# Optimization experiments

Measured on AMD Instinct MI355X. Metric: run time of the kernel, lower is better.

Reference implementation:

```python
import jax, jax.numpy as jnp
import numpy as np

N = 50000      # nodes
E = 800000     # edges (before self-loops)
F_IN = 256
H = 8          # heads layer 1
C = 64         # hidden channels per head
OUT = 40       # classes
NEG_SLOPE = 0.2


def setup_inputs() -> dict:
    key = jax.random.key(0)
    ks = jax.random.split(key, 10)
    sc = 0.05
    return {
        "x": jax.random.normal(ks[0], (N, F_IN), jnp.float32),
        "edge_index": jax.random.randint(ks[1], (2, E), 0, N, dtype=jnp.int64),
        "W1": jax.random.normal(ks[2], (F_IN, H * C), jnp.float32) * sc,
        "a_src1": jax.random.normal(ks[3], (H, C), jnp.float32) * sc,
        "a_dst1": jax.random.normal(ks[4], (H, C), jnp.float32) * sc,
        "b1": jnp.zeros((H * C,), jnp.float32),
        "W2": jax.random.normal(ks[5], (H * C, OUT), jnp.float32) * sc,
        "a_src2": jax.random.normal(ks[6], (1, OUT), jnp.float32) * sc,
        "a_dst2": jax.random.normal(ks[7], (1, OUT), jnp.float32) * sc,
        "b2": jnp.zeros((OUT,), jnp.float32),
    }


def gat_layer(h_in, src, dst, W, a_s, a_d, b, heads, ch, concat, n):
    # h: [n, heads, ch] per-head linear transform
    h = (h_in @ W).reshape(n, heads, ch)
    alpha_s = jnp.sum(h * a_s, axis=-1)   # [n, heads]
    alpha_d = jnp.sum(h * a_d, axis=-1)   # [n, heads]
    # edge-wise raw attention logits [E, heads]
    e = jax.nn.leaky_relu(alpha_s[src] + alpha_d[dst], NEG_SLOPE)
    # segment softmax over incoming edges of each dst node
    m = jax.ops.segment_max(e, dst, num_segments=n)
    w = jnp.exp(e - m[dst])
    s = jax.ops.segment_sum(w, dst, num_segments=n)
    alpha = w / s[dst]                    # [E, heads]
    # scatter-aggregate messages: [n, heads, ch]
    out = jax.ops.segment_sum(h[src] * alpha[:, :, None], dst, num_segments=n)
    out = out.reshape(n, heads * ch) if concat else out.mean(axis=1)
    return out + b


def reference(x, edge_index, W1, a_src1, a_dst1, b1, W2, a_src2, a_dst2, b2):
    # add self-loops (PyG GATConv default); guarantees every dst has >=1 edge
    loop = jnp.arange(N, dtype=edge_index.dtype)
    src = jnp.concatenate([edge_index[0], loop])
    dst = jnp.concatenate([edge_index[1], loop])
    h = gat_layer(x, src, dst, W1, a_src1, a_dst1, b1, H, C, True, N)
    h = jax.nn.relu(h)  # dropout is identity in eval mode
    out = gat_layer(h, src, dst, W2, a_src2, a_dst2, b2, 1, OUT, False, N)
    return jax.nn.log_softmax(out, axis=1)
```

## Files before the change

kernel.cpp:

```cpp
#include <hip/hip_runtime.h>

#define N_NODES 50000
#define N_EDGES 800000
#define F_INK   256
#define HC      512
#define OUT_C   40
#define OUT_P   48
#define NEG     0.2f
#define CAP     64
#define GEMM_NB 782
#define CHUNKS  782
#define PART_SZ 6250
#define SCAT_NB (CHUNKS * 8)

typedef short short8 __attribute__((ext_vector_type(8)));
typedef float f32x4 __attribute__((ext_vector_type(4)));
typedef float f32x2 __attribute__((ext_vector_type(2)));

__device__ __forceinline__ float bf2f(unsigned short u) {
    union { unsigned int i; float f; } v; v.i = ((unsigned int)u) << 16; return v.f;
}
__device__ __forceinline__ unsigned short f2bf(float f) {
    union { float f; unsigned int i; } v; v.f = f;
    unsigned int x = v.i;
    return (unsigned short)((x + 0x7fffu + ((x >> 16) & 1u)) >> 16);
}
__device__ __forceinline__ float bflo(unsigned int u) {
    union { unsigned int i; float f; } v; v.i = u << 16; return v.f;
}
__device__ __forceinline__ float bfhi(unsigned int u) {
    union { unsigned int i; float f; } v; v.i = u & 0xffff0000u; return v.f;
}
__device__ __forceinline__ bool ei_is64(const int* ei) {
    return ei[1] == 0 && ei[3] == 0 && ei[5] == 0;
}
__device__ __forceinline__ float lrelu(float x) { return fmaxf(x, NEG * x); }
__device__ __forceinline__ unsigned char f2fp8(float v) {
    return (unsigned char)(__builtin_amdgcn_cvt_pk_fp8_f32(v, v, 0, false) & 0xff);
}
__device__ __forceinline__ float fp82f(unsigned char b) {
    f32x2 p = __builtin_amdgcn_cvt_pk_f32_fp8((int)b, false);
    return p[0];
}

__global__ __launch_bounds__(256) void prep_k(const float* __restrict__ W1, const float* __restrict__ W2,
                       const float* __restrict__ s1, const float* __restrict__ d1, const float* __restrict__ b1,
                       const float* __restrict__ s2, const float* __restrict__ d2, const float* __restrict__ b2,
                       unsigned short* __restrict__ W1p, unsigned short* __restrict__ W2p,
                       unsigned short* __restrict__ s1c, unsigned short* __restrict__ d1c,
                       unsigned short* __restrict__ b1c, unsigned short* __restrict__ s2c,
                       unsigned short* __restrict__ d2c, unsigned short* __restrict__ b2c,
                       int* __restrict__ cnt) {
    int b = blockIdx.x;
    if (b < 512) {
        int t = b * 256 + threadIdx.x;
        int k = t / HC, n = t % HC;
        int s = k >> 5, q = (k >> 3) & 3, j = k & 7;
        W1p[((((s << 2) + q) * HC + n) << 3) + j] = f2bf(W1[k * HC + n]);
    } else if (b < 608) {
        int t = (b - 512) * 256 + threadIdx.x;
        int k = t / OUT_P, n = t % OUT_P;
        int s = k >> 5, q = (k >> 3) & 3, j = k & 7;
        unsigned short v = (n < OUT_C) ? f2bf(W2[k * OUT_C + n]) : (unsigned short)0;
        W2p[((((s << 2) + q) * OUT_P + n) << 3) + j] = v;
    } else if (b == 608) {
        int t = threadIdx.x;
        for (int j = t; j < 512; j += 256) {
            s1c[j] = f2bf(s1[j]); d1c[j] = f2bf(d1[j]); b1c[j] = f2bf(b1[j]);
        }
        if (t < OUT_C) { s2c[t] = f2bf(s2[t]); d2c[t] = f2bf(d2[t]); b2c[t] = f2bf(b2[t]); }
    } else {
        int i = (b - 609) * 256 + threadIdx.x;
        if (i < N_NODES) cnt[i * 16] = 0;
    }
}

__global__ __launch_bounds__(256) void gemm1_k(const float* __restrict__ x,
                                               const unsigned short* __restrict__ Wp,
                                               const unsigned short* __restrict__ a_s,
                                               const unsigned short* __restrict__ a_d,
                                               unsigned char* __restrict__ h1f8,
                                               float* __restrict__ as1, float* __restrict__ ad1,
                                               const int* __restrict__ ei,
                                               int* __restrict__ cnt, int* __restrict__ srcs) {
    __shared__ unsigned short xs[64 * 264];
    int tid = threadIdx.x;
    if (blockIdx.x >= GEMM_NB) {
        int sb = blockIdx.x - GEMM_NB;
        int part = blockIdx.x & 7;
        int chunk = sb >> 3;
        int lo = part * PART_SZ;
        bool is64 = ei_is64(ei);
        int e0 = chunk * 1024 + (tid << 2);
        int s[4], d[4];
        bool vld[4];
        if (chunk < CHUNKS - 1) {
            if (is64) {
                int4 a0 = *reinterpret_cast<const int4*>(ei + 2 * e0);
                int4 a1 = *reinterpret_cast<const int4*>(ei + 2 * e0 + 4);
                int4 c0 = *reinterpret_cast<const int4*>(ei + 2 * N_EDGES + 2 * e0);
                int4 c1 = *reinterpret_cast<const int4*>(ei + 2 * N_EDGES + 2 * e0 + 4);
                s[0] = a0.x; s[1] = a0.z; s[2] = a1.x; s[3] = a1.z;
                d[0] = c0.x; d[1] = c0.z; d[2] = c1.x; d[3] = c1.z;
            } else {
                int4 a0 = *reinterpret_cast<const int4*>(ei + e0);
                int4 c0 = *reinterpret_cast<const int4*>(ei + N_EDGES + e0);
                s[0] = a0.x; s[1] = a0.y; s[2] = a0.z; s[3] = a0.w;
                d[0] = c0.x; d[1] = c0.y; d[2] = c0.z; d[3] = c0.w;
            }
            vld[0] = vld[1] = vld[2] = vld[3] = true;
        } else {
#pragma unroll
            for (int j = 0; j < 4; j++) {
                int e = e0 + j;
                vld[j] = e < N_EDGES;
                int ec = vld[j] ? e : 0;
                s[j] = is64 ? ei[2 * ec] : ei[ec];
                d[j] = is64 ? ei[2 * N_EDGES + 2 * ec] : ei[N_EDGES + ec];
            }
        }
#pragma unroll
        for (int j = 0; j < 4; j++) {
            int dj = d[j];
            if (vld[j] && dj >= lo && dj < lo + PART_SZ) {
                int pos = atomicAdd(&cnt[dj * 16], 1);
                if (pos < CAP) srcs[(size_t)dj * CAP + pos] = s[j];
            }
        }
        return;
    }
    int bm = blockIdx.x;
    int row0 = bm * 64;
#pragma unroll
    for (int it = 0; it < 16; it++) {
        int j = tid + it * 256;
        int r = j >> 6;
        int c = (j & 63) << 2;
        int rr = row0 + r; rr = rr < N_NODES ? rr : N_NODES - 1;
        float4 f = *reinterpret_cast<const float4*>(x + (size_t)rr * F_INK + c);
        unsigned int lo = (unsigned int)f2bf(f.x) | ((unsigned int)f2bf(f.y) << 16);
        unsigned int hi = (unsigned int)f2bf(f.z) | ((unsigned int)f2bf(f.w) << 16);
        *reinterpret_cast<uint2*>(&xs[r * 264 + c]) = make_uint2(lo, hi);
    }
    __syncthreads();
    int w = tid >> 6, lane = tid & 63;
    int q = lane >> 4, l16 = lane & 15;
    short8 a[8];
#pragma unroll
    for (int s = 0; s < 8; s++)
        a[s] = *reinterpret_cast<const short8*>(&xs[(w * 16 + l16) * 264 + s * 32 + q * 8]);
    int orow = row0 + w * 16 + q * 4;
#pragma unroll
    for (int bn = 0; bn < 8; bn++) {
        f32x4 acc[4];
#pragma unroll
        for (int t = 0; t < 4; t++) acc[t] = (f32x4){0.f, 0.f, 0.f, 0.f};
#pragma unroll
        for (int s = 0; s < 8; s++) {
#pragma unroll
            for (int t = 0; t < 4; t++) {
                int col = bn * 64 + t * 16 + l16;
                short8 b = *reinterpret_cast<const short8*>(Wp + ((((s << 2) + q) * HC + col) << 3));
                acc[t] = __builtin_amdgcn_mfma_f32_16x16x32_bf16(a[s], b, acc[t], 0, 0, 0);
            }
        }
        float sa0 = 0.f, sa1 = 0.f, sa2 = 0.f, sa3 = 0.f;
        float da0 = 0.f, da1 = 0.f, da2 = 0.f, da3 = 0.f;
#pragma unroll
        for (int t = 0; t < 4; t++) {
            int col = bn * 64 + t * 16 + l16;
            float asc = bf2f(a_s[col]);
            float adc = bf2f(a_d[col]);
            float v0 = acc[t][0], v1 = acc[t][1], v2 = acc[t][2], v3 = acc[t][3];
            sa0 += v0 * asc; da0 += v0 * adc;
            sa1 += v1 * asc; da1 += v1 * adc;
            sa2 += v2 * asc; da2 += v2 * adc;
            sa3 += v3 * asc; da3 += v3 * adc;
            if (orow + 3 < N_NODES) {
                h1f8[(size_t)(orow + 0) * HC + col] = f2fp8(v0);
                h1f8[(size_t)(orow + 1) * HC + col] = f2fp8(v1);
                h1f8[(size_t)(orow + 2) * HC + col] = f2fp8(v2);
                h1f8[(size_t)(orow + 3) * HC + col] = f2fp8(v3);
            } else {
                if (orow + 0 < N_NODES) h1f8[(size_t)(orow + 0) * HC + col] = f2fp8(v0);
                if (orow + 1 < N_NODES) h1f8[(size_t)(orow + 1) * HC + col] = f2fp8(v1);
                if (orow + 2 < N_NODES) h1f8[(size_t)(orow + 2) * HC + col] = f2fp8(v2);
                if (orow + 3 < N_NODES) h1f8[(size_t)(orow + 3) * HC + col] = f2fp8(v3);
            }
        }
#pragma unroll
        for (int m = 1; m < 16; m <<= 1) {
            sa0 += __shfl_xor(sa0, m, 64); sa1 += __shfl_xor(sa1, m, 64);
            sa2 += __shfl_xor(sa2, m, 64); sa3 += __shfl_xor(sa3, m, 64);
            da0 += __shfl_xor(da0, m, 64); da1 += __shfl_xor(da1, m, 64);
            da2 += __shfl_xor(da2, m, 64); da3 += __shfl_xor(da3, m, 64);
        }
        if (l16 < 4) {
            int rr = orow + l16;
            float sav = (l16 == 0) ? sa0 : (l16 == 1) ? sa1 : (l16 == 2) ? sa2 : sa3;
            float dav = (l16 == 0) ? da0 : (l16 == 1) ? da1 : (l16 == 2) ? da2 : da3;
            if (rr < N_NODES) { as1[rr * 8 + bn] = sav; ad1[rr * 8 + bn] = dav; }
        }
    }
}

#define ACC16(u, wgt)                                                              \
    {                                                                              \
        f32x2 q0 = __builtin_amdgcn_cvt_pk_f32_fp8((int)(u).x, false);             \
        f32x2 q1 = __builtin_amdgcn_cvt_pk_f32_fp8((int)(u).x, true);              \
        f32x2 q2 = __builtin_amdgcn_cvt_pk_f32_fp8((int)(u).y, false);             \
        f32x2 q3 = __builtin_amdgcn_cvt_pk_f32_fp8((int)(u).y, true);              \
        f32x2 q4 = __builtin_amdgcn_cvt_pk_f32_fp8((int)(u).z, false);             \
        f32x2 q5 = __builtin_amdgcn_cvt_pk_f32_fp8((int)(u).z, true);              \
        f32x2 q6 = __builtin_amdgcn_cvt_pk_f32_fp8((int)(u).w, false);             \
        f32x2 q7 = __builtin_amdgcn_cvt_pk_f32_fp8((int)(u).w, true);              \
        f32x2 wv = {(wgt), (wgt)};                                                 \
        ac[0] += wv * q0; ac[1] += wv * q1; ac[2] += wv * q2; ac[3] += wv * q3;    \
        ac[4] += wv * q4; ac[5] += wv * q5; ac[6] += wv * q6; ac[7] += wv * q7;    \
    }

__global__ __launch_bounds__(256) void agg1_k(const unsigned char* __restrict__ h1f8,
                                              const float* __restrict__ as1,
                                              const float* __restrict__ ad1,
                                              const int* __restrict__ cnt,
                                              const int* __restrict__ srcs,
                                              const unsigned short* __restrict__ b1,
                                              const unsigned short* __restrict__ W2p,
                                              const unsigned short* __restrict__ a_s2,
                                              const unsigned short* __restrict__ a_d2,
                                              unsigned char* __restrict__ h2f8) {
    __shared__ unsigned short rows[16 * 520];
    __shared__ int sSrc[16 * CAP];
    __shared__ int sCnt[16];
    __shared__ float sAs[16], sAd[16];
    __shared__ int ctr;
    int tid = threadIdx.x;
    int base = blockIdx.x * 16;
    reinterpret_cast<int4*>(sSrc)[tid] =
        reinterpret_cast<const int4*>(srcs + (size_t)base * CAP)[tid];
    if (tid < 16) {
        int d = cnt[(base + tid) * 16];
        sCnt[tid] = d < CAP ? d : CAP;
        sAs[tid] = 0.f; sAd[tid] = 0.f;
    }
    if (tid == 0) ctr = 0;
    __syncthreads();
    int w = tid >> 6, lane = tid & 63;
    int half = lane >> 5, li = lane & 31;
    int h = li >> 2;
    uint4 ub0 = reinterpret_cast<const uint4*>(b1)[li * 2 + 0];
    uint4 ub1 = reinterpret_cast<const uint4*>(b1)[li * 2 + 1];
    for (;;) {
        int rl = 0;
        if (lane == 0) rl = atomicAdd(&ctr, 1);
        rl = __shfl(rl, 0, 64);
        if (rl >= 16) break;
        int wid = base + rl;
        float adv = ad1[wid * 8 + h];
        const int* sp = sSrc + rl * CAP;
        int deg = sCnt[rl];
        f32x2 ac[8];
#pragma unroll
        for (int k = 0; k < 8; k++) ac[k] = (f32x2){0.f, 0.f};
        float sumw = 0.f;
        {
            int s = half ? (deg > 0 ? sp[0] : wid) : wid;
            float A = as1[s * 8 + h];
            uint4 u = reinterpret_cast<const uint4*>(h1f8 + (size_t)s * HC)[li];
            float wj = (half && deg == 0) ? 0.f : __expf(lrelu(A + adv));
            sumw += wj;
            ACC16(u, wj)
        }
        int v = 1;
        for (; v + 16 <= deg; v += 16) {
            int s[8]; float A[8]; uint4 u[8];
#pragma unroll
            for (int j = 0; j < 8; j++) s[j] = sp[v + 2 * j + half];
#pragma unroll
            for (int j = 0; j < 8; j++) A[j] = as1[s[j] * 8 + h];
#pragma unroll
            for (int j = 0; j < 8; j++)
                u[j] = reinterpret_cast<const uint4*>(h1f8 + (size_t)s[j] * HC)[li];
#pragma unroll
            for (int j = 0; j < 8; j++) {
                float wj = __expf(lrelu(A[j] + adv));
                sumw += wj;
                ACC16(u[j], wj)
            }
        }
        for (; v + 8 <= deg; v += 8) {
            int s[4]; float A[4]; uint4 u[4];
#pragma unroll
            for (int j = 0; j < 4; j++) s[j] = sp[v + 2 * j + half];
#pragma unroll
            for (int j = 0; j < 4; j++) A[j] = as1[s[j] * 8 + h];
#pragma unroll
            for (int j = 0; j < 4; j++)
                u[j] = reinterpret_cast<const uint4*>(h1f8 + (size_t)s[j] * HC)[li];
#pragma unroll
            for (int j = 0; j < 4; j++) {
                float wj = __expf(lrelu(A[j] + adv));
                sumw += wj;
                ACC16(u[j], wj)
            }
        }
        for (; v + 4 <= deg; v += 4) {
            int s[2]; float A[2]; uint4 u[2];
#pragma unroll
            for (int j = 0; j < 2; j++) s[j] = sp[v + 2 * j + half];
#pragma unroll
            for (int j = 0; j < 2; j++) A[j] = as1[s[j] * 8 + h];
#pragma unroll
            for (int j = 0; j < 2; j++)
                u[j] = reinterpret_cast<const uint4*>(h1f8 + (size_t)s[j] * HC)[li];
#pragma unroll
            for (int j = 0; j < 2; j++) {
                float wj = __expf(lrelu(A[j] + adv));
                sumw += wj;
                ACC16(u[j], wj)
            }
        }
        for (; v < deg; v += 2) {
            int vv = v + half;
            bool ok = vv < deg;
            int s = ok ? sp[vv] : wid;
            float A = as1[s * 8 + h];
            uint4 u = reinterpret_cast<const uint4*>(h1f8 + (size_t)s * HC)[li];
            float wj = ok ? __expf(lrelu(A + adv)) : 0.f;
            sumw += wj;
            ACC16(u, wj)
        }
        sumw += __shfl_xor(sumw, 32, 64);
#pragma unroll
        for (int k = 0; k < 8; k++) {
            ac[k][0] += __shfl_xor(ac[k][0], 32, 64);
            ac[k][1] += __shfl_xor(ac[k][1], 32, 64);
        }
        float inv = 1.f / sumw;
        f32x2 n0 = half ? ac[4] : ac[0];
        f32x2 n1 = half ? ac[5] : ac[1];
        f32x2 n2 = half ? ac[6] : ac[2];
        f32x2 n3 = half ? ac[7] : ac[3];
        uint4 ubh = half ? ub1 : ub0;
        float o0 = fmaxf(n0[0] * inv + bflo(ubh.x), 0.f);
        float o1 = fmaxf(n0[1] * inv + bfhi(ubh.x), 0.f);
        float o2 = fmaxf(n1[0] * inv + bflo(ubh.y), 0.f);
        float o3 = fmaxf(n1[1] * inv + bfhi(ubh.y), 0.f);
        float o4 = fmaxf(n2[0] * inv + bflo(ubh.z), 0.f);
        float o5 = fmaxf(n2[1] * inv + bfhi(ubh.z), 0.f);
        float o6 = fmaxf(n3[0] * inv + bflo(ubh.w), 0.f);
        float o7 = fmaxf(n3[1] * inv + bfhi(ubh.w), 0.f);
        uint4 r;
        r.x = (unsigned int)f2bf(o0) | ((unsigned int)f2bf(o1) << 16);
        r.y = (unsigned int)f2bf(o2) | ((unsigned int)f2bf(o3) << 16);
        r.z = (unsigned int)f2bf(o4) | ((unsigned int)f2bf(o5) << 16);
        r.w = (unsigned int)f2bf(o6) | ((unsigned int)f2bf(o7) << 16);
        *reinterpret_cast<uint4*>(&rows[rl * 520 + li * 16 + half * 8]) = r;
    }
    __syncthreads();
    if (w < 3) {
        int q = lane >> 4, l16 = lane & 15;
        int col = w * 16 + l16;
        f32x4 acc = (f32x4){0.f, 0.f, 0.f, 0.f};
#pragma unroll
        for (int s = 0; s < HC / 32; s++) {
            short8 a = *reinterpret_cast<const short8*>(&rows[l16 * 520 + s * 32 + q * 8]);
            short8 b = *reinterpret_cast<const short8*>(W2p + ((((s << 2) + q) * OUT_P + col) << 3));
            acc = __builtin_amdgcn_mfma_f32_16x16x32_bf16(a, b, acc, 0, 0, 0);
        }
        float sa0 = 0.f, sa1 = 0.f, sa2 = 0.f, sa3 = 0.f;
        float da0 = 0.f, da1 = 0.f, da2 = 0.f, da3 = 0.f;
        if (col < OUT_C) {
            float asc = bf2f(a_s2[col]);
            float adc = bf2f(a_d2[col]);
            sa0 = acc[0] * asc; da0 = acc[0] * adc;
            sa1 = acc[1] * asc; da1 = acc[1] * adc;
            sa2 = acc[2] * asc; da2 = acc[2] * adc;
            sa3 = acc[3] * asc; da3 = acc[3] * adc;
#pragma unroll
            for (int r = 0; r < 4; r++)
                h2f8[(size_t)(base + q * 4 + r) * 64 + col] = f2fp8(acc[r]);
        }
#pragma unroll
        for (int m = 1; m < 16; m <<= 1) {
            sa0 += __shfl_xor(sa0, m, 64); sa1 += __shfl_xor(sa1, m, 64);
            sa2 += __shfl_xor(sa2, m, 64); sa3 += __shfl_xor(sa3, m, 64);
            da0 += __shfl_xor(da0, m, 64); da1 += __shfl_xor(da1, m, 64);
            da2 += __shfl_xor(da2, m, 64); da3 += __shfl_xor(da3, m, 64);
        }
        if (l16 < 4) {
            int rr = q * 4 + l16;
            float sav = (l16 == 0) ? sa0 : (l16 == 1) ? sa1 : (l16 == 2) ? sa2 : sa3;
            float dav = (l16 == 0) ? da0 : (l16 == 1) ? da1 : (l16 == 2) ? da2 : da3;
            atomicAdd(&sAs[rr], sav);
            atomicAdd(&sAd[rr], dav);
        }
    }
    __syncthreads();
    if (tid < 16) {
        unsigned char* r = h2f8 + (size_t)(base + tid) * 64;
        *reinterpret_cast<float*>(r + 40) = sAs[tid];
        *reinterpret_cast<float*>(r + 44) = sAd[tid];
    }
}

__global__ __launch_bounds__(256) void agg2_k(const unsigned char* __restrict__ h2f8,
                                              const int* __restrict__ cnt,
                                              const int* __restrict__ srcs,
                                              const unsigned short* __restrict__ b2,
                                              float* __restrict__ outp) {
    int wid = blockIdx.x * 4 + (threadIdx.x >> 6);
    if (wid >= N_NODES) return;
    int lane = threadIdx.x & 63;
    bool act = lane < OUT_C;
    int lclamp = act ? lane : 0;
    const unsigned char* rd = h2f8 + (size_t)wid * 64;
    float adv = *reinterpret_cast<const float*>(rd + 44);
    float acc, sumw;
    {
        float w0 = __expf(lrelu(*reinterpret_cast<const float*>(rd + 40) + adv));
        sumw = w0;
        acc = w0 * fp82f(rd[lclamp]);
    }
    int deg = cnt[wid * 16]; deg = deg < CAP ? deg : CAP;
    int e = wid * CAP, e1 = e + deg;
    for (; e + 4 <= e1; e += 4) {
        int s0 = srcs[e], s1 = srcs[e + 1], s2 = srcs[e + 2], s3 = srcs[e + 3];
        const unsigned char* r0 = h2f8 + (size_t)s0 * 64;
        const unsigned char* r1 = h2f8 + (size_t)s1 * 64;
        const unsigned char* r2 = h2f8 + (size_t)s2 * 64;
        const unsigned char* r3 = h2f8 + (size_t)s3 * 64;
        float A0 = *reinterpret_cast<const float*>(r0 + 40);
        float A1 = *reinterpret_cast<const float*>(r1 + 40);
        float A2 = *reinterpret_cast<const float*>(r2 + 40);
        float A3 = *reinterpret_cast<const float*>(r3 + 40);
        unsigned char c0 = r0[lclamp];
        unsigned char c1 = r1[lclamp];
        unsigned char c2 = r2[lclamp];
        unsigned char c3 = r3[lclamp];
        float w0 = __expf(lrelu(A0 + adv));
        float w1 = __expf(lrelu(A1 + adv));
        float w2 = __expf(lrelu(A2 + adv));
        float w3 = __expf(lrelu(A3 + adv));
        sumw += (w0 + w1) + (w2 + w3);
        acc += w0 * fp82f(c0) + w1 * fp82f(c1) + w2 * fp82f(c2) + w3 * fp82f(c3);
    }
    for (; e < e1; e++) {
        int s0 = srcs[e];
        const unsigned char* r0 = h2f8 + (size_t)s0 * 64;
        float w0 = __expf(lrelu(*reinterpret_cast<const float*>(r0 + 40) + adv));
        sumw += w0;
        acc += w0 * fp82f(r0[lclamp]);
    }
    float o = acc / sumw + bf2f(b2[lclamp]);
    float mval = act ? o : -1e30f;
#pragma unroll
    for (int m = 32; m >= 1; m >>= 1) mval = fmaxf(mval, __shfl_xor(mval, m, 64));
    float ex = act ? __expf(o - mval) : 0.f;
#pragma unroll
    for (int m = 32; m >= 1; m >>= 1) ex += __shfl_xor(ex, m, 64);
    float res = o - mval - __logf(ex);
    if (act) outp[(size_t)wid * OUT_C + lane] = res;
}

extern "C" void kernel_launch(void* const* d_in, const int* in_sizes, int n_in,
                              void* d_out, int out_size, void* d_ws, size_t ws_size,
                              hipStream_t stream) {
    const float* x      = (const float*)d_in[0];
    const int*   ei     = (const int*)d_in[1];
    const float* W1     = (const float*)d_in[2];
    const float* as1raw = (const float*)d_in[3];
    const float* ad1raw = (const float*)d_in[4];
    const float* b1raw  = (const float*)d_in[5];
    const float* W2     = (const float*)d_in[6];
    const float* as2raw = (const float*)d_in[7];
    const float* ad2raw = (const float*)d_in[8];
    const float* b2raw  = (const float*)d_in[9];
    float* out = (float*)d_out;

    char* p = (char*)d_ws;
    auto alloc = [&](size_t bytes) -> char* {
        char* r = p;
        p += (bytes + 255) & ~(size_t)255;
        return r;
    };
    unsigned short* s1c  = (unsigned short*)alloc(512 * 2);
    unsigned short* d1c  = (unsigned short*)alloc(512 * 2);
    unsigned short* b1c  = (unsigned short*)alloc(512 * 2);
    unsigned short* s2c  = (unsigned short*)alloc(OUT_C * 2);
    unsigned short* d2c  = (unsigned short*)alloc(OUT_C * 2);
    unsigned short* b2c  = (unsigned short*)alloc(OUT_C * 2);
    unsigned char*  h1f8 = (unsigned char*)alloc((size_t)N_NODES * HC);
    unsigned char*  h2f8 = (unsigned char*)alloc((size_t)N_NODES * 64);
    float* as1  = (float*)alloc((size_t)N_NODES * 8 * 4);
    float* ad1  = (float*)alloc((size_t)N_NODES * 8 * 4);
    int* cnt    = (int*)alloc((size_t)N_NODES * 64);
    int* srcs   = (int*)alloc((size_t)N_NODES * CAP * 4);
    unsigned short* W1p = (unsigned short*)alloc((size_t)F_INK * HC * 2);
    unsigned short* W2p = (unsigned short*)alloc((size_t)HC * OUT_P * 2);
    (void)ws_size; (void)in_sizes; (void)n_in; (void)out_size;

    const int NB = (N_NODES + 255) / 256;

    prep_k<<<609 + NB, 256, 0, stream>>>(W1, W2, as1raw, ad1raw, b1raw, as2raw, ad2raw, b2raw,
                                         W1p, W2p, s1c, d1c, b1c, s2c, d2c, b2c, cnt);
    gemm1_k<<<GEMM_NB + SCAT_NB, 256, 0, stream>>>(x, W1p, s1c, d1c, h1f8, as1, ad1,
                                                   ei, cnt, srcs);
    agg1_k<<<N_NODES / 16, 256, 0, stream>>>(h1f8, as1, ad1, cnt, srcs, b1c,
                                             W2p, s2c, d2c, h2f8);
    agg2_k<<<(N_NODES + 3) / 4, 256, 0, stream>>>(h2f8, cnt, srcs, b2c, out);
}
```

Baseline: 273.0 us.

## Split edge scatter into its own kernel and stage source lists in LDS for agg2

Moves the edge bucketing (atomic scatter into per-destination source lists) out of the fused GEMM launch into a separate scat_k kernel, so GEMM blocks no longer share a grid with scatter blocks. The layer-2 aggregation now loads each block's four source lists and degrees into shared memory with one cooperative vectorized load, then gathers neighbor rows eight at a time to raise memory-level parallelism. The split adds a kernel launch and gives up the overlap between GEMM and scatter that the fused grid allowed.

```diff
diff --git a/kernel.cpp b/kernel.cpp
--- a/kernel.cpp
+++ b/kernel.cpp
@@ -75,60 +75,59 @@
     }
 }
 
+__global__ __launch_bounds__(256) void scat_k(const int* __restrict__ ei,
+                                              int* __restrict__ cnt, int* __restrict__ srcs) {
+    int tid = threadIdx.x;
+    int part = blockIdx.x & 7;
+    int chunk = blockIdx.x >> 3;
+    int lo = part * PART_SZ;
+    bool is64 = ei_is64(ei);
+    int e0 = chunk * 1024 + (tid << 2);
+    int s[4], d[4];
+    bool vld[4];
+    if (chunk < CHUNKS - 1) {
+        if (is64) {
+            int4 a0 = *reinterpret_cast<const int4*>(ei + 2 * e0);
+            int4 a1 = *reinterpret_cast<const int4*>(ei + 2 * e0 + 4);
+            int4 c0 = *reinterpret_cast<const int4*>(ei + 2 * N_EDGES + 2 * e0);
+            int4 c1 = *reinterpret_cast<const int4*>(ei + 2 * N_EDGES + 2 * e0 + 4);
+            s[0] = a0.x; s[1] = a0.z; s[2] = a1.x; s[3] = a1.z;
+            d[0] = c0.x; d[1] = c0.z; d[2] = c1.x; d[3] = c1.z;
+        } else {
+            int4 a0 = *reinterpret_cast<const int4*>(ei + e0);
+            int4 c0 = *reinterpret_cast<const int4*>(ei + N_EDGES + e0);
+            s[0] = a0.x; s[1] = a0.y; s[2] = a0.z; s[3] = a0.w;
+            d[0] = c0.x; d[1] = c0.y; d[2] = c0.z; d[3] = c0.w;
+        }
+        vld[0] = vld[1] = vld[2] = vld[3] = true;
+    } else {
+#pragma unroll
+        for (int j = 0; j < 4; j++) {
+            int e = e0 + j;
+            vld[j] = e < N_EDGES;
+            int ec = vld[j] ? e : 0;
+            s[j] = is64 ? ei[2 * ec] : ei[ec];
+            d[j] = is64 ? ei[2 * N_EDGES + 2 * ec] : ei[N_EDGES + ec];
+        }
+    }
+#pragma unroll
+    for (int j = 0; j < 4; j++) {
+        int dj = d[j];
+        if (vld[j] && dj >= lo && dj < lo + PART_SZ) {
+            int pos = atomicAdd(&cnt[dj * 16], 1);
+            if (pos < CAP) srcs[(size_t)dj * CAP + pos] = s[j];
+        }
+    }
+}
+
 __global__ __launch_bounds__(256) void gemm1_k(const float* __restrict__ x,
                                                const unsigned short* __restrict__ Wp,
                                                const unsigned short* __restrict__ a_s,
                                                const unsigned short* __restrict__ a_d,
                                                unsigned char* __restrict__ h1f8,
-                                               float* __restrict__ as1, float* __restrict__ ad1,
-                                               const int* __restrict__ ei,
-                                               int* __restrict__ cnt, int* __restrict__ srcs) {
+                                               float* __restrict__ as1, float* __restrict__ ad1) {
     __shared__ unsigned short xs[64 * 264];
     int tid = threadIdx.x;
-    if (blockIdx.x >= GEMM_NB) {
-        int sb = blockIdx.x - GEMM_NB;
-        int part = blockIdx.x & 7;
-        int chunk = sb >> 3;
-        int lo = part * PART_SZ;
-        bool is64 = ei_is64(ei);
-        int e0 = chunk * 1024 + (tid << 2);
-        int s[4], d[4];
-        bool vld[4];
-        if (chunk < CHUNKS - 1) {
-            if (is64) {
-                int4 a0 = *reinterpret_cast<const int4*>(ei + 2 * e0);
-                int4 a1 = *reinterpret_cast<const int4*>(ei + 2 * e0 + 4);
-                int4 c0 = *reinterpret_cast<const int4*>(ei + 2 * N_EDGES + 2 * e0);
-                int4 c1 = *reinterpret_cast<const int4*>(ei + 2 * N_EDGES + 2 * e0 + 4);
-                s[0] = a0.x; s[1] = a0.z; s[2] = a1.x; s[3] = a1.z;
-                d[0] = c0.x; d[1] = c0.z; d[2] = c1.x; d[3] = c1.z;
-            } else {
-                int4 a0 = *reinterpret_cast<const int4*>(ei + e0);
-                int4 c0 = *reinterpret_cast<const int4*>(ei + N_EDGES + e0);
-                s[0] = a0.x; s[1] = a0.y; s[2] = a0.z; s[3] = a0.w;
-                d[0] = c0.x; d[1] = c0.y; d[2] = c0.z; d[3] = c0.w;
-            }
-            vld[0] = vld[1] = vld[2] = vld[3] = true;
-        } else {
-#pragma unroll
-            for (int j = 0; j < 4; j++) {
-                int e = e0 + j;
-                vld[j] = e < N_EDGES;
-                int ec = vld[j] ? e : 0;
-                s[j] = is64 ? ei[2 * ec] : ei[ec];
-                d[j] = is64 ? ei[2 * N_EDGES + 2 * ec] : ei[N_EDGES + ec];
-            }
-        }
-#pragma unroll
-        for (int j = 0; j < 4; j++) {
-            int dj = d[j];
-            if (vld[j] && dj >= lo && dj < lo + PART_SZ) {
-                int pos = atomicAdd(&cnt[dj * 16], 1);
-                if (pos < CAP) srcs[(size_t)dj * CAP + pos] = s[j];
-            }
-        }
-        return;
-    }
     int bm = blockIdx.x;
     int row0 = bm * 64;
 #pragma unroll
@@ -409,9 +408,21 @@
                                               const int* __restrict__ srcs,
                                               const unsigned short* __restrict__ b2,
                                               float* __restrict__ outp) {
-    int wid = blockIdx.x * 4 + (threadIdx.x >> 6);
-    if (wid >= N_NODES) return;
-    int lane = threadIdx.x & 63;
+    __shared__ int sSrc[4 * CAP];
+    __shared__ int sCnt[4];
+    int tid = threadIdx.x;
+    int base = blockIdx.x * 4;
+    if (tid < 64)
+        reinterpret_cast<int4*>(sSrc)[tid] =
+            reinterpret_cast<const int4*>(srcs + (size_t)base * CAP)[tid];
+    if (tid < 4) {
+        int d = cnt[(base + tid) * 16];
+        sCnt[tid] = d < CAP ? d : CAP;
+    }
+    __syncthreads();
+    int w = tid >> 6;
+    int wid = base + w;
+    int lane = tid & 63;
     bool act = lane < OUT_C;
     int lclamp = act ? lane : 0;
     const unsigned char* rd = h2f8 + (size_t)wid * 64;
@@ -422,32 +433,45 @@
         sumw = w0;
         acc = w0 * fp82f(rd[lclamp]);
     }
-    int deg = cnt[wid * 16]; deg = deg < CAP ? deg : CAP;
-    int e = wid * CAP, e1 = e + deg;
-    for (; e + 4 <= e1; e += 4) {
-        int s0 = srcs[e], s1 = srcs[e + 1], s2 = srcs[e + 2], s3 = srcs[e + 3];
-        const unsigned char* r0 = h2f8 + (size_t)s0 * 64;
-        const unsigned char* r1 = h2f8 + (size_t)s1 * 64;
-        const unsigned char* r2 = h2f8 + (size_t)s2 * 64;
-        const unsigned char* r3 = h2f8 + (size_t)s3 * 64;
-        float A0 = *reinterpret_cast<const float*>(r0 + 40);
-        float A1 = *reinterpret_cast<const float*>(r1 + 40);
-        float A2 = *reinterpret_cast<const float*>(r2 + 40);
-        float A3 = *reinterpret_cast<const float*>(r3 + 40);
-        unsigned char c0 = r0[lclamp];
-        unsigned char c1 = r1[lclamp];
-        unsigned char c2 = r2[lclamp];
-        unsigned char c3 = r3[lclamp];
-        float w0 = __expf(lrelu(A0 + adv));
-        float w1 = __expf(lrelu(A1 + adv));
-        float w2 = __expf(lrelu(A2 + adv));
-        float w3 = __expf(lrelu(A3 + adv));
-        sumw += (w0 + w1) + (w2 + w3);
-        acc += w0 * fp82f(c0) + w1 * fp82f(c1) + w2 * fp82f(c2) + w3 * fp82f(c3);
-    }
-    for (; e < e1; e++) {
-        int s0 = srcs[e];
-        const unsigned char* r0 = h2f8 + (size_t)s0 * 64;
+    const int* sp = sSrc + w * CAP;
+    int deg = sCnt[w];
+    int v = 0;
+    for (; v + 8 <= deg; v += 8) {
+        const unsigned char* r[8];
+        float A[8];
+        unsigned char c[8];
+#pragma unroll
+        for (int j = 0; j < 8; j++) r[j] = h2f8 + (size_t)sp[v + j] * 64;
+#pragma unroll
+        for (int j = 0; j < 8; j++) A[j] = *reinterpret_cast<const float*>(r[j] + 40);
+#pragma unroll
+        for (int j = 0; j < 8; j++) c[j] = r[j][lclamp];
+#pragma unroll
+        for (int j = 0; j < 8; j++) {
+            float wj = __expf(lrelu(A[j] + adv));
+            sumw += wj;
+            acc += wj * fp82f(c[j]);
+        }
+    }
+    for (; v + 4 <= deg; v += 4) {
+        const unsigned char* r[4];
+        float A[4];
+        unsigned char c[4];
+#pragma unroll
+        for (int j = 0; j < 4; j++) r[j] = h2f8 + (size_t)sp[v + j] * 64;
+#pragma unroll
+        for (int j = 0; j < 4; j++) A[j] = *reinterpret_cast<const float*>(r[j] + 40);
+#pragma unroll
+        for (int j = 0; j < 4; j++) c[j] = r[j][lclamp];
+#pragma unroll
+        for (int j = 0; j < 4; j++) {
+            float wj = __expf(lrelu(A[j] + adv));
+            sumw += wj;
+            acc += wj * fp82f(c[j]);
+        }
+    }
+    for (; v < deg; v++) {
+        const unsigned char* r0 = h2f8 + (size_t)sp[v] * 64;
         float w0 = __expf(lrelu(*reinterpret_cast<const float*>(r0 + 40) + adv));
         sumw += w0;
         acc += w0 * fp82f(r0[lclamp]);
@@ -504,9 +528,9 @@
 
     prep_k<<<609 + NB, 256, 0, stream>>>(W1, W2, as1raw, ad1raw, b1raw, as2raw, ad2raw, b2raw,
                                          W1p, W2p, s1c, d1c, b1c, s2c, d2c, b2c, cnt);
-    gemm1_k<<<GEMM_NB + SCAT_NB, 256, 0, stream>>>(x, W1p, s1c, d1c, h1f8, as1, ad1,
-                                                   ei, cnt, srcs);
+    gemm1_k<<<GEMM_NB, 256, 0, stream>>>(x, W1p, s1c, d1c, h1f8, as1, ad1);
+    scat_k<<<SCAT_NB, 256, 0, stream>>>(ei, cnt, srcs);
     agg1_k<<<N_NODES / 16, 256, 0, stream>>>(h1f8, as1, ad1, cnt, srcs, b1c,
                                              W2p, s2c, d2c, h2f8);
-    agg2_k<<<(N_NODES + 3) / 4, 256, 0, stream>>>(h2f8, cnt, srcs, b2c, out);
-}
+    agg2_k<<<N_NODES / 4, 256, 0, stream>>>(h2f8, cnt, srcs, b2c, out);
+}
```

Measured after the change: 290.2 us. 1.06x slower.
